# Kernel optimization log

Hardware: AMD Instinct MI355X
Metric: run time of the kernel (lower is better)

## Reference

```python
import jax, jax.numpy as jnp
import numpy as np

B, S, D, H = 2, 2048, 1024, 16
DK = D // H


def setup_inputs() -> dict:
    key = jax.random.key(0)
    ks = jax.random.split(key, 7)
    x = jax.random.normal(ks[0], (B, S, D), dtype=jnp.float32)
    gamma = jax.random.normal(ks[1], (D,), dtype=jnp.float32)
    mask = jax.random.randint(ks[2], (B, S), 0, 2, dtype=jnp.int32)
    w_qkv_w = jax.random.normal(ks[3], (D, 3 * D), dtype=jnp.float32) / np.sqrt(D)
    w_qkv_b = jax.random.normal(ks[4], (3 * D,), dtype=jnp.float32) * 0.02
    w_o_w = jax.random.normal(ks[5], (D, D), dtype=jnp.float32) / np.sqrt(D)
    w_o_b = jax.random.normal(ks[6], (D,), dtype=jnp.float32) * 0.02
    return {"x": x, "gamma": gamma, "mask": mask, "w_qkv_w": w_qkv_w,
            "w_qkv_b": w_qkv_b, "w_o_w": w_o_w, "w_o_b": w_o_b}


def reference(x, gamma, mask, w_qkv_w, w_qkv_b, w_o_w, w_o_b):
    b, s, d = x.shape
    # QKV projection, then per-head interleaved chunk (matches torch view+chunk)
    qkv = x @ w_qkv_w + w_qkv_b                      # [B,S,3D]
    qkv = qkv.reshape(b, s, H, 3 * DK).transpose(0, 2, 1, 3)  # [B,H,S,3*dk]
    q, k, v = jnp.split(qkv, 3, axis=-1)             # each [B,H,S,dk]
    scale = 1.0 / np.sqrt(DK).astype(np.float32)
    scores = jnp.einsum('bhqd,bhkd->bhqk', q, k) * scale  # [B,H,S,S]
    m = mask[:, None, None, :]                       # 2D mask -> [B,1,1,S]
    scores = jnp.where(m == 0, -jnp.inf, scores)
    attn = jax.nn.softmax(scores, axis=-1)           # dropout p=0.0 -> identity
    out = jnp.einsum('bhqk,bhkd->bhqd', attn, v)     # [B,H,S,dk]
    out = out.transpose(0, 2, 1, 3).reshape(b, s, d) # [B,S,D]
    out = out @ w_o_w + w_o_b
    return (gamma + 1.0) * out
```

## Files before the change

kernel.cpp:

```cpp
#include <hip/hip_runtime.h>
#include <hip/hip_bf16.h>


using bf16 = __hip_bfloat16;
typedef __attribute__((ext_vector_type(8))) short bf16x8;
typedef __attribute__((ext_vector_type(4))) float f32x4;

#define QSCALE 0.18033688011112042f

static __device__ __forceinline__ f32x4 mfma_bf16(bf16x8 a, bf16x8 b, f32x4 c) {
    return __builtin_amdgcn_mfma_f32_16x16x32_bf16(a, b, c, 0, 0, 0);
}

static __device__ __forceinline__ void gld_lds16(const void* g, void* s) {
    __builtin_amdgcn_global_load_lds(
        (const __attribute__((address_space(1))) unsigned int*)g,
        (__attribute__((address_space(3))) unsigned int*)s,
        16, 0, 0);
}

__global__ void cast_bf16_kernel(const float* __restrict__ in, bf16* __restrict__ out, int n4) {
    int i = blockIdx.x * blockDim.x + threadIdx.x;
    if (i >= n4) return;
    float4 f = reinterpret_cast<const float4*>(in)[i];
    out[4*i+0] = __float2bfloat16(f.x);
    out[4*i+1] = __float2bfloat16(f.y);
    out[4*i+2] = __float2bfloat16(f.z);
    out[4*i+3] = __float2bfloat16(f.w);
}

__global__ void transpose_cast_kernel(const float* __restrict__ in, bf16* __restrict__ out,
                                      int R, int C) {
    __shared__ float tile[32][33];
    int c0 = blockIdx.x * 32, r0 = blockIdx.y * 32;
    int x = threadIdx.x, y = threadIdx.y;
#pragma unroll
    for (int i = 0; i < 32; i += 8) tile[y + i][x] = in[(size_t)(r0 + y + i) * C + c0 + x];
    __syncthreads();
#pragma unroll
    for (int i = 0; i < 32; i += 8)
        out[(size_t)(c0 + y + i) * R + r0 + x] = __float2bfloat16(tile[x][y + i]);
}

template <int EPI>
__global__ __launch_bounds__(256, 2)
void gemm_bt_kernel(const bf16* __restrict__ A, const bf16* __restrict__ Bt,
                    int M, int N, int K,
                    const float* __restrict__ bias, const float* __restrict__ gamma,
                    bf16* __restrict__ Qout, bf16* __restrict__ Kout, bf16* __restrict__ Vtout,
                    float* __restrict__ Cout) {
    __shared__ __align__(16) bf16 As[128 * 64];
    __shared__ __align__(16) bf16 Bs[128 * 64];

    const int tid  = threadIdx.x;
    const int wave = tid >> 6, lane = tid & 63;
    const int quad = lane >> 4, l16 = lane & 15;
    const int wr = wave >> 1, wc = wave & 1;
    const int bm = blockIdx.y, bn = blockIdx.x;

    f32x4 acc[4][4] = {};

    const int crow = lane >> 3;
    const int sblk = (lane & 7) ^ (crow & 7);
    const bf16* gA[4]; const bf16* gB[4]; bf16* lA[4]; bf16* lB[4];
#pragma unroll
    for (int c = 0; c < 4; ++c) {
        int rt = wave * 32 + c * 8 + crow;
        gA[c] = A  + (size_t)(bm * 128 + rt) * K + sblk * 8;
        gB[c] = Bt + (size_t)(bn * 128 + rt) * K + sblk * 8;
        lA[c] = As + (wave * 4 + c) * 512 + lane * 8;
        lB[c] = Bs + (wave * 4 + c) * 512 + lane * 8;
    }
    const int xr = l16 & 7;

    for (int k0 = 0; k0 < K; k0 += 64) {
#pragma unroll
        for (int c = 0; c < 4; ++c) gld_lds16(gA[c] + k0, lA[c]);
#pragma unroll
        for (int c = 0; c < 4; ++c) gld_lds16(gB[c] + k0, lB[c]);
        __syncthreads();
#pragma unroll
        for (int ks = 0; ks < 2; ++ks) {
            bf16x8 af[4], bfr[4];
#pragma unroll
            for (int mi = 0; mi < 4; ++mi)
                af[mi] = *(const bf16x8*)(As + (wr * 64 + mi * 16 + l16) * 64 + ((4 * ks + quad) ^ xr) * 8);
#pragma unroll
            for (int ni = 0; ni < 4; ++ni)
                bfr[ni] = *(const bf16x8*)(Bs + (wc * 64 + ni * 16 + l16) * 64 + ((4 * ks + quad) ^ xr) * 8);
#pragma unroll
            for (int mi = 0; mi < 4; ++mi)
#pragma unroll
                for (int ni = 0; ni < 4; ++ni)
                    acc[mi][ni] = mfma_bf16(af[mi], bfr[ni], acc[mi][ni]);
        }
        __syncthreads();
    }

#pragma unroll
    for (int mi = 0; mi < 4; ++mi) {
#pragma unroll
        for (int ni = 0; ni < 4; ++ni) {
#pragma unroll
            for (int r = 0; r < 4; ++r) {
                int row = bm * 128 + wr * 64 + mi * 16 + quad * 4 + r;
                int col = bn * 128 + wc * 64 + ni * 16 + l16;
                float v = acc[mi][ni][r];
                if (EPI == 0) {
                    v += bias[col];
                    int h = col / 192;
                    int rr = col - h * 192;
                    int which = rr >> 6, dk = rr & 63;
                    int b = row >> 11, s = row & 2047;
                    size_t bh = (size_t)b * 16 + h;
                    if (which == 0) {
                        Qout[(bh * 2048 + s) * 64 + dk] = __float2bfloat16(v * QSCALE);
                    } else if (which == 1) {
                        Kout[(bh * 2048 + s) * 64 + dk] = __float2bfloat16(v);
                    } else {
                        Vtout[(bh * 64 + dk) * 2048 + s] = __float2bfloat16(v);
                    }
                } else {
                    float o = (gamma[col] + 1.0f) * (v + bias[col]);
                    Cout[(size_t)row * N + col] = o;
                }
            }
        }
    }
}

__global__ __launch_bounds__(256, 2)
void attn_kernel(const bf16* __restrict__ Qb, const bf16* __restrict__ Kb,
                 const bf16* __restrict__ Vt, const int* __restrict__ mask,
                 bf16* __restrict__ Aout) {
    __shared__ __align__(16) bf16 Ks[64 * 72];
    __shared__ __align__(16) bf16 Vs[64 * 72];
    __shared__ __align__(16) bf16 Ps[4][32 * 72];
    __shared__ float Biass[64];

    const int bh = blockIdx.y;
    const int b = bh >> 4, h = bh & 15;
    const int q0 = blockIdx.x * 128;
    const int tid = threadIdx.x;
    const int wave = tid >> 6, lane = tid & 63;
    const int quad = lane >> 4, l16 = lane & 15;

    bf16x8 aq[2][2];
#pragma unroll
    for (int m = 0; m < 2; ++m) {
        const bf16* qp = Qb + ((size_t)bh * 2048 + q0 + wave * 32 + m * 16 + l16) * 64;
        aq[m][0] = *(const bf16x8*)(qp + quad * 8);
        aq[m][1] = *(const bf16x8*)(qp + 32 + quad * 8);
    }

    bf16x8 ones;
#pragma unroll
    for (int j = 0; j < 8; ++j) ones[j] = (short)0x3F80;

    f32x4 O[2][4] = {};
    f32x4 Lacc[2] = {};

    const int srow = tid >> 2, spart = tid & 3;
    const bf16* gK = Kb + ((size_t)bh * 2048 + srow) * 64 + spart * 16;
    const bf16* gV = Vt + ((size_t)bh * 64 + srow) * 2048 + spart * 16;
    uint4* lK = (uint4*)(Ks + srow * 72 + spart * 16);
    uint4* lV = (uint4*)(Vs + srow * 72 + spart * 16);
    bf16* myPs = &Ps[wave][0];

    uint4 kr0, kr1, vr0, vr1; int mreg = 1;
    {
        const uint4* nk = (const uint4*)gK;
        const uint4* nv = (const uint4*)gV;
        kr0 = nk[0]; kr1 = nk[1];
        vr0 = nv[0]; vr1 = nv[1];
        if (tid < 64) mreg = mask[b * 2048 + tid];
    }

    for (int kt = 0; kt < 32; ++kt) {
        lK[0] = kr0; lK[1] = kr1;
        lV[0] = vr0; lV[1] = vr1;
        if (tid < 64) Biass[tid] = mreg ? -24.0f : -1e30f;
        __syncthreads();

        if (kt + 1 < 32) {
            const uint4* nk = (const uint4*)(gK + (size_t)(kt + 1) * 64 * 64);
            const uint4* nv = (const uint4*)(gV + (kt + 1) * 64);
            kr0 = nk[0]; kr1 = nk[1];
            vr0 = nv[0]; vr1 = nv[1];
            if (tid < 64) mreg = mask[b * 2048 + (kt + 1) * 64 + tid];
        }

        float bv4[4];
        bf16x8 bk[4][2];
#pragma unroll
        for (int nt = 0; nt < 4; ++nt) {
            bv4[nt] = Biass[nt * 16 + l16];
            const bf16* kp = Ks + (nt * 16 + l16) * 72 + quad * 8;
            bk[nt][0] = *(const bf16x8*)kp;
            bk[nt][1] = *(const bf16x8*)(kp + 32);
        }

#pragma unroll
        for (int m = 0; m < 2; ++m) {
#pragma unroll
            for (int nt = 0; nt < 4; ++nt) {
                f32x4 c = {0.f, 0.f, 0.f, 0.f};
                c = mfma_bf16(aq[m][0], bk[nt][0], c);
                c = mfma_bf16(aq[m][1], bk[nt][1], c);
#pragma unroll
                for (int r = 0; r < 4; ++r) {
                    float p = __builtin_amdgcn_exp2f(c[r] + bv4[nt]);
                    myPs[(m * 16 + quad * 4 + r) * 72 + nt * 16 + l16] = __float2bfloat16(p);
                }
            }
        }

#pragma unroll
        for (int m = 0; m < 2; ++m) {
#pragma unroll
            for (int ks = 0; ks < 2; ++ks) {
                bf16x8 ap = *(const bf16x8*)(myPs + (m * 16 + l16) * 72 + ks * 32 + quad * 8);
                Lacc[m] = mfma_bf16(ap, ones, Lacc[m]);
#pragma unroll
                for (int nt = 0; nt < 4; ++nt) {
                    bf16x8 bvv = *(const bf16x8*)(Vs + (nt * 16 + l16) * 72 + ks * 32 + quad * 8);
                    O[m][nt] = mfma_bf16(ap, bvv, O[m][nt]);
                }
            }
        }
        __syncthreads();
    }

#pragma unroll
    for (int m = 0; m < 2; ++m) {
        float inv[4];
#pragma unroll
        for (int r = 0; r < 4; ++r) inv[r] = __builtin_amdgcn_rcpf(Lacc[m][r]);
#pragma unroll
        for (int nt = 0; nt < 4; ++nt) {
#pragma unroll
            for (int r = 0; r < 4; ++r) {
                int row = q0 + wave * 32 + m * 16 + quad * 4 + r;
                Aout[((size_t)b * 2048 + row) * 1024 + h * 64 + nt * 16 + l16] =
                    __float2bfloat16(O[m][nt][r] * inv[r]);
            }
        }
    }
}

extern "C" void kernel_launch(void* const* d_in, const int* in_sizes, int n_in,
                              void* d_out, int out_size, void* d_ws, size_t ws_size,
                              hipStream_t stream) {
    const float* x     = (const float*)d_in[0];
    const float* gamma = (const float*)d_in[1];
    const int*   mask  = (const int*)d_in[2];
    const float* wqkv  = (const float*)d_in[3];
    const float* bqkv  = (const float*)d_in[4];
    const float* wo    = (const float*)d_in[5];
    const float* bo    = (const float*)d_in[6];
    float* out = (float*)d_out;

    char* ws = (char*)d_ws;
    const size_t MB = 1u << 20;
    bf16* xb    = (bf16*)(ws);
    bf16* wqkvT = (bf16*)(ws + 8 * MB);
    bf16* woT   = (bf16*)(ws + 14 * MB);
    bf16* Qb    = (bf16*)(ws + 16 * MB);
    bf16* Kb    = (bf16*)(ws + 24 * MB);
    bf16* Vt    = (bf16*)(ws + 32 * MB);
    bf16* attn  = (bf16*)(ws + 40 * MB);

    cast_bf16_kernel<<<4096, 256, 0, stream>>>(x, xb, 4194304 / 4);
    transpose_cast_kernel<<<dim3(96, 32), dim3(32, 8), 0, stream>>>(wqkv, wqkvT, 1024, 3072);
    transpose_cast_kernel<<<dim3(32, 32), dim3(32, 8), 0, stream>>>(wo, woT, 1024, 1024);

    gemm_bt_kernel<0><<<dim3(24, 32), 256, 0, stream>>>(
        xb, wqkvT, 4096, 3072, 1024, bqkv, nullptr, Qb, Kb, Vt, nullptr);

    attn_kernel<<<dim3(16, 32), 256, 0, stream>>>(Qb, Kb, Vt, mask, attn);

    gemm_bt_kernel<1><<<dim3(8, 32), 256, 0, stream>>>(
        attn, woT, 4096, 1024, 1024, bo, gamma, nullptr, nullptr, nullptr, out);
}
```

Baseline: 211.9 us.

## Stream K/V tiles via global_load_lds with XOR swizzle and separate V transpose

The QKV GEMM now writes V row-major, and a new kernel transposes it into Vt; this replaces the strided scattered transposed stores in the GEMM epilogue. The attention kernel loads K and V tiles straight into LDS with global_load_lds using an XOR swizzle instead of padded rows. It keeps P in fp32 LDS and packs to bf16 when reading, and hoists the V fragment loads out of the inner loop. The cost is an extra kernel launch and another round trip of V through memory. The register prefetch of the next tile is dropped, so loads are no longer overlapped with compute, and fp32 P doubles its LDS footprint.

```diff
diff --git a/kernel.cpp b/kernel.cpp
--- a/kernel.cpp
+++ b/kernel.cpp
@@ -17,6 +17,17 @@
         (const __attribute__((address_space(1))) unsigned int*)g,
         (__attribute__((address_space(3))) unsigned int*)s,
         16, 0, 0);
+}
+
+static __device__ __forceinline__ short f2s(float f) {
+    bf16 h = __float2bfloat16(f);
+    return *reinterpret_cast<short*>(&h);
+}
+static __device__ __forceinline__ bf16x8 pack8(float4 a, float4 b) {
+    bf16x8 r;
+    r[0] = f2s(a.x); r[1] = f2s(a.y); r[2] = f2s(a.z); r[3] = f2s(a.w);
+    r[4] = f2s(b.x); r[5] = f2s(b.y); r[6] = f2s(b.z); r[7] = f2s(b.w);
+    return r;
 }
 
 __global__ void cast_bf16_kernel(const float* __restrict__ in, bf16* __restrict__ out, int n4) {
@@ -42,12 +53,29 @@
         out[(size_t)(c0 + y + i) * R + r0 + x] = __float2bfloat16(tile[x][y + i]);
 }
 
+__global__ void transpose_v_kernel(const bf16* __restrict__ in, bf16* __restrict__ out) {
+    __shared__ bf16 t[64][72];
+    const int bh = blockIdx.y, s0 = blockIdx.x * 64;
+    const int r = threadIdx.x >> 2, c16 = (threadIdx.x & 3) * 16;
+    const uint4* src = (const uint4*)(in + ((size_t)bh * 2048 + s0 + r) * 64 + c16);
+    uint4 a = src[0], b = src[1];
+    *(uint4*)&t[r][c16] = a;
+    *(uint4*)&t[r][c16 + 8] = b;
+    __syncthreads();
+    bf16 tmp[16];
+#pragma unroll
+    for (int i = 0; i < 16; ++i) tmp[i] = t[c16 + i][r];
+    uint4* dst = (uint4*)(out + ((size_t)bh * 64 + r) * 2048 + s0 + c16);
+    dst[0] = ((uint4*)tmp)[0];
+    dst[1] = ((uint4*)tmp)[1];
+}
+
 template <int EPI>
 __global__ __launch_bounds__(256, 2)
 void gemm_bt_kernel(const bf16* __restrict__ A, const bf16* __restrict__ Bt,
                     int M, int N, int K,
                     const float* __restrict__ bias, const float* __restrict__ gamma,
-                    bf16* __restrict__ Qout, bf16* __restrict__ Kout, bf16* __restrict__ Vtout,
+                    bf16* __restrict__ Qout, bf16* __restrict__ Kout, bf16* __restrict__ Vout,
                     float* __restrict__ Cout) {
     __shared__ __align__(16) bf16 As[128 * 64];
     __shared__ __align__(16) bf16 Bs[128 * 64];
@@ -118,7 +146,7 @@
                     } else if (which == 1) {
                         Kout[(bh * 2048 + s) * 64 + dk] = __float2bfloat16(v);
                     } else {
-                        Vtout[(bh * 64 + dk) * 2048 + s] = __float2bfloat16(v);
+                        Vout[(bh * 2048 + s) * 64 + dk] = __float2bfloat16(v);
                     }
                 } else {
                     float o = (gamma[col] + 1.0f) * (v + bias[col]);
@@ -133,9 +161,9 @@
 void attn_kernel(const bf16* __restrict__ Qb, const bf16* __restrict__ Kb,
                  const bf16* __restrict__ Vt, const int* __restrict__ mask,
                  bf16* __restrict__ Aout) {
-    __shared__ __align__(16) bf16 Ks[64 * 72];
-    __shared__ __align__(16) bf16 Vs[64 * 72];
-    __shared__ __align__(16) bf16 Ps[4][32 * 72];
+    __shared__ __align__(16) bf16 Ks[64 * 64];
+    __shared__ __align__(16) bf16 Vs[64 * 64];
+    __shared__ __align__(16) float Psf[4][32 * 68];
     __shared__ float Biass[64];
 
     const int bh = blockIdx.y;
@@ -144,6 +172,7 @@
     const int tid = threadIdx.x;
     const int wave = tid >> 6, lane = tid & 63;
     const int quad = lane >> 4, l16 = lane & 15;
+    const int xr = l16 & 7;
 
     bf16x8 aq[2][2];
 #pragma unroll
@@ -160,44 +189,40 @@
     f32x4 O[2][4] = {};
     f32x4 Lacc[2] = {};
 
-    const int srow = tid >> 2, spart = tid & 3;
-    const bf16* gK = Kb + ((size_t)bh * 2048 + srow) * 64 + spart * 16;
-    const bf16* gV = Vt + ((size_t)bh * 64 + srow) * 2048 + spart * 16;
-    uint4* lK = (uint4*)(Ks + srow * 72 + spart * 16);
-    uint4* lV = (uint4*)(Vs + srow * 72 + spart * 16);
-    bf16* myPs = &Ps[wave][0];
-
-    uint4 kr0, kr1, vr0, vr1; int mreg = 1;
-    {
-        const uint4* nk = (const uint4*)gK;
-        const uint4* nv = (const uint4*)gV;
-        kr0 = nk[0]; kr1 = nk[1];
-        vr0 = nv[0]; vr1 = nv[1];
-        if (tid < 64) mreg = mask[b * 2048 + tid];
-    }
+    const int crow = lane >> 3;
+    const int sblk = (lane & 7) ^ (crow & 7);
+    const bf16* gK[2]; const bf16* gV[2]; bf16* lK[2]; bf16* lV[2];
+#pragma unroll
+    for (int c = 0; c < 2; ++c) {
+        int ch = wave * 2 + c;
+        gK[c] = Kb + ((size_t)bh * 2048 + ch * 8 + crow) * 64 + sblk * 8;
+        gV[c] = Vt + ((size_t)bh * 64 + ch * 8 + crow) * 2048 + sblk * 8;
+        lK[c] = Ks + ch * 512 + lane * 8;
+        lV[c] = Vs + ch * 512 + lane * 8;
+    }
+    float* myP = &Psf[wave][0];
+
+    int mreg = (tid < 64) ? mask[b * 2048 + tid] : 0;
 
     for (int kt = 0; kt < 32; ++kt) {
-        lK[0] = kr0; lK[1] = kr1;
-        lV[0] = vr0; lV[1] = vr1;
+#pragma unroll
+        for (int c = 0; c < 2; ++c) {
+            gld_lds16(gK[c] + (size_t)kt * 4096, lK[c]);
+            gld_lds16(gV[c] + kt * 64, lV[c]);
+        }
         if (tid < 64) Biass[tid] = mreg ? -24.0f : -1e30f;
         __syncthreads();
 
-        if (kt + 1 < 32) {
-            const uint4* nk = (const uint4*)(gK + (size_t)(kt + 1) * 64 * 64);
-            const uint4* nv = (const uint4*)(gV + (kt + 1) * 64);
-            kr0 = nk[0]; kr1 = nk[1];
-            vr0 = nv[0]; vr1 = nv[1];
-            if (tid < 64) mreg = mask[b * 2048 + (kt + 1) * 64 + tid];
-        }
+        if (kt + 1 < 32 && tid < 64) mreg = mask[b * 2048 + (kt + 1) * 64 + tid];
 
         float bv4[4];
         bf16x8 bk[4][2];
 #pragma unroll
         for (int nt = 0; nt < 4; ++nt) {
             bv4[nt] = Biass[nt * 16 + l16];
-            const bf16* kp = Ks + (nt * 16 + l16) * 72 + quad * 8;
-            bk[nt][0] = *(const bf16x8*)kp;
-            bk[nt][1] = *(const bf16x8*)(kp + 32);
+            const bf16* kp = Ks + (nt * 16 + l16) * 64;
+            bk[nt][0] = *(const bf16x8*)(kp + ((quad) ^ xr) * 8);
+            bk[nt][1] = *(const bf16x8*)(kp + ((quad + 4) ^ xr) * 8);
         }
 
 #pragma unroll
@@ -207,25 +232,31 @@
                 f32x4 c = {0.f, 0.f, 0.f, 0.f};
                 c = mfma_bf16(aq[m][0], bk[nt][0], c);
                 c = mfma_bf16(aq[m][1], bk[nt][1], c);
-#pragma unroll
-                for (int r = 0; r < 4; ++r) {
-                    float p = __builtin_amdgcn_exp2f(c[r] + bv4[nt]);
-                    myPs[(m * 16 + quad * 4 + r) * 72 + nt * 16 + l16] = __float2bfloat16(p);
-                }
+                float* pw = myP + (m * 16 + quad * 4) * 68 + nt * 16 + l16;
+#pragma unroll
+                for (int r = 0; r < 4; ++r)
+                    pw[r * 68] = __builtin_amdgcn_exp2f(c[r] + bv4[nt]);
             }
         }
 
+        bf16x8 bv[2][4];
+#pragma unroll
+        for (int ks = 0; ks < 2; ++ks)
+#pragma unroll
+            for (int nt = 0; nt < 4; ++nt)
+                bv[ks][nt] = *(const bf16x8*)(Vs + (nt * 16 + l16) * 64 + ((quad + 4 * ks) ^ xr) * 8);
+
 #pragma unroll
         for (int m = 0; m < 2; ++m) {
 #pragma unroll
             for (int ks = 0; ks < 2; ++ks) {
-                bf16x8 ap = *(const bf16x8*)(myPs + (m * 16 + l16) * 72 + ks * 32 + quad * 8);
+                const float4* pp = (const float4*)(myP + (m * 16 + l16) * 68 + ks * 32 + quad * 8);
+                float4 p0 = pp[0], p1 = pp[1];
+                bf16x8 ap = pack8(p0, p1);
                 Lacc[m] = mfma_bf16(ap, ones, Lacc[m]);
 #pragma unroll
-                for (int nt = 0; nt < 4; ++nt) {
-                    bf16x8 bvv = *(const bf16x8*)(Vs + (nt * 16 + l16) * 72 + ks * 32 + quad * 8);
-                    O[m][nt] = mfma_bf16(ap, bvv, O[m][nt]);
-                }
+                for (int nt = 0; nt < 4; ++nt)
+                    O[m][nt] = mfma_bf16(ap, bv[ks][nt], O[m][nt]);
             }
         }
         __syncthreads();
@@ -268,6 +299,7 @@
     bf16* Qb    = (bf16*)(ws + 16 * MB);
     bf16* Kb    = (bf16*)(ws + 24 * MB);
     bf16* Vt    = (bf16*)(ws + 32 * MB);
+    bf16* Vtmp  = (bf16*)(ws + 40 * MB);
     bf16* attn  = (bf16*)(ws + 40 * MB);
 
     cast_bf16_kernel<<<4096, 256, 0, stream>>>(x, xb, 4194304 / 4);
@@ -275,7 +307,9 @@
     transpose_cast_kernel<<<dim3(32, 32), dim3(32, 8), 0, stream>>>(wo, woT, 1024, 1024);
 
     gemm_bt_kernel<0><<<dim3(24, 32), 256, 0, stream>>>(
-        xb, wqkvT, 4096, 3072, 1024, bqkv, nullptr, Qb, Kb, Vt, nullptr);
+        xb, wqkvT, 4096, 3072, 1024, bqkv, nullptr, Qb, Kb, Vtmp, nullptr);
+
+    transpose_v_kernel<<<dim3(32, 32), 256, 0, stream>>>(Vtmp, Vt);
 
     attn_kernel<<<dim3(16, 32), 256, 0, stream>>>(Qb, Kb, Vt, mask, attn);
 
```

Result: no change. 215.5 us (+1.7%).

## Keep attention probabilities in registers and add separate V transpose kernel

Applied to the files above, without the earlier changes.

The attention kernel now computes S^T by swapping MFMA operands, so the exp'd probabilities already sit in the register layout needed as the A operand of the PV MFMA. This removes the per-wave LDS round trip for P and frees that shared memory. V fragments are gathered with 4-element loads from a padded LDS layout. Separately, the QKV GEMM now writes V row-major with coalesced stores and a new small kernel transposes it to V^T, which adds a launch and extra memory traffic in exchange for removing the strided scatter in the GEMM epilogue.

```diff
diff --git a/kernel.cpp b/kernel.cpp
--- a/kernel.cpp
+++ b/kernel.cpp
@@ -4,6 +4,7 @@
 
 using bf16 = __hip_bfloat16;
 typedef __attribute__((ext_vector_type(8))) short bf16x8;
+typedef __attribute__((ext_vector_type(4))) short bf16x4;
 typedef __attribute__((ext_vector_type(4))) float f32x4;
 
 #define QSCALE 0.18033688011112042f
@@ -17,6 +18,11 @@
         (const __attribute__((address_space(1))) unsigned int*)g,
         (__attribute__((address_space(3))) unsigned int*)s,
         16, 0, 0);
+}
+
+static __device__ __forceinline__ short f2s(float f) {
+    bf16 h = __float2bfloat16(f);
+    return *reinterpret_cast<short*>(&h);
 }
 
 __global__ void cast_bf16_kernel(const float* __restrict__ in, bf16* __restrict__ out, int n4) {
@@ -42,12 +48,29 @@
         out[(size_t)(c0 + y + i) * R + r0 + x] = __float2bfloat16(tile[x][y + i]);
 }
 
+__global__ void transpose_v_kernel(const bf16* __restrict__ in, bf16* __restrict__ out) {
+    __shared__ bf16 t[64][72];
+    const int bh = blockIdx.y, s0 = blockIdx.x * 64;
+    const int r = threadIdx.x >> 2, c16 = (threadIdx.x & 3) * 16;
+    const uint4* src = (const uint4*)(in + ((size_t)bh * 2048 + s0 + r) * 64 + c16);
+    uint4 a = src[0], b = src[1];
+    *(uint4*)&t[r][c16] = a;
+    *(uint4*)&t[r][c16 + 8] = b;
+    __syncthreads();
+    bf16 tmp[16];
+#pragma unroll
+    for (int i = 0; i < 16; ++i) tmp[i] = t[c16 + i][r];
+    uint4* dst = (uint4*)(out + ((size_t)bh * 64 + r) * 2048 + s0 + c16);
+    dst[0] = ((uint4*)tmp)[0];
+    dst[1] = ((uint4*)tmp)[1];
+}
+
 template <int EPI>
 __global__ __launch_bounds__(256, 2)
 void gemm_bt_kernel(const bf16* __restrict__ A, const bf16* __restrict__ Bt,
                     int M, int N, int K,
                     const float* __restrict__ bias, const float* __restrict__ gamma,
-                    bf16* __restrict__ Qout, bf16* __restrict__ Kout, bf16* __restrict__ Vtout,
+                    bf16* __restrict__ Qout, bf16* __restrict__ Kout, bf16* __restrict__ Vout,
                     float* __restrict__ Cout) {
     __shared__ __align__(16) bf16 As[128 * 64];
     __shared__ __align__(16) bf16 Bs[128 * 64];
@@ -118,7 +141,7 @@
                     } else if (which == 1) {
                         Kout[(bh * 2048 + s) * 64 + dk] = __float2bfloat16(v);
                     } else {
-                        Vtout[(bh * 64 + dk) * 2048 + s] = __float2bfloat16(v);
+                        Vout[(bh * 2048 + s) * 64 + dk] = __float2bfloat16(v);
                     }
                 } else {
                     float o = (gamma[col] + 1.0f) * (v + bias[col]);
@@ -134,9 +157,8 @@
                  const bf16* __restrict__ Vt, const int* __restrict__ mask,
                  bf16* __restrict__ Aout) {
     __shared__ __align__(16) bf16 Ks[64 * 72];
-    __shared__ __align__(16) bf16 Vs[64 * 72];
-    __shared__ __align__(16) bf16 Ps[4][32 * 72];
-    __shared__ float Biass[64];
+    __shared__ __align__(16) bf16 Vs[64 * 76];
+    __shared__ __align__(16) float Biass[64];
 
     const int bh = blockIdx.y;
     const int b = bh >> 4, h = bh & 15;
@@ -164,8 +186,7 @@
     const bf16* gK = Kb + ((size_t)bh * 2048 + srow) * 64 + spart * 16;
     const bf16* gV = Vt + ((size_t)bh * 64 + srow) * 2048 + spart * 16;
     uint4* lK = (uint4*)(Ks + srow * 72 + spart * 16);
-    uint4* lV = (uint4*)(Vs + srow * 72 + spart * 16);
-    bf16* myPs = &Ps[wave][0];
+    uint4* lV = (uint4*)(Vs + srow * 76 + spart * 16);
 
     uint4 kr0, kr1, vr0, vr1; int mreg = 1;
     {
@@ -190,42 +211,58 @@
             if (tid < 64) mreg = mask[b * 2048 + (kt + 1) * 64 + tid];
         }
 
-        float bv4[4];
+        f32x4 bias4[4];
         bf16x8 bk[4][2];
 #pragma unroll
-        for (int nt = 0; nt < 4; ++nt) {
-            bv4[nt] = Biass[nt * 16 + l16];
-            const bf16* kp = Ks + (nt * 16 + l16) * 72 + quad * 8;
-            bk[nt][0] = *(const bf16x8*)kp;
-            bk[nt][1] = *(const bf16x8*)(kp + 32);
+        for (int kt4 = 0; kt4 < 4; ++kt4) {
+            bias4[kt4] = *(const f32x4*)(Biass + kt4 * 16 + quad * 4);
+            const bf16* kp = Ks + (kt4 * 16 + l16) * 72 + quad * 8;
+            bk[kt4][0] = *(const bf16x8*)kp;
+            bk[kt4][1] = *(const bf16x8*)(kp + 32);
+        }
+        bf16x8 bv8[2][4];
+#pragma unroll
+        for (int a = 0; a < 2; ++a) {
+#pragma unroll
+            for (int nt = 0; nt < 4; ++nt) {
+                const bf16* vp = Vs + (nt * 16 + l16) * 76 + a * 32 + quad * 4;
+                bf16x4 lo = *(const bf16x4*)vp;
+                bf16x4 hi = *(const bf16x4*)(vp + 16);
+                bf16x8 f;
+                f[0] = lo[0]; f[1] = lo[1]; f[2] = lo[2]; f[3] = lo[3];
+                f[4] = hi[0]; f[5] = hi[1]; f[6] = hi[2]; f[7] = hi[3];
+                bv8[a][nt] = f;
+            }
         }
 
 #pragma unroll
         for (int m = 0; m < 2; ++m) {
-#pragma unroll
-            for (int nt = 0; nt < 4; ++nt) {
+            f32x4 sv[4];
+#pragma unroll
+            for (int kt4 = 0; kt4 < 4; ++kt4) {
                 f32x4 c = {0.f, 0.f, 0.f, 0.f};
-                c = mfma_bf16(aq[m][0], bk[nt][0], c);
-                c = mfma_bf16(aq[m][1], bk[nt][1], c);
-#pragma unroll
-                for (int r = 0; r < 4; ++r) {
-                    float p = __builtin_amdgcn_exp2f(c[r] + bv4[nt]);
-                    myPs[(m * 16 + quad * 4 + r) * 72 + nt * 16 + l16] = __float2bfloat16(p);
-                }
-            }
-        }
-
-#pragma unroll
-        for (int m = 0; m < 2; ++m) {
-#pragma unroll
-            for (int ks = 0; ks < 2; ++ks) {
-                bf16x8 ap = *(const bf16x8*)(myPs + (m * 16 + l16) * 72 + ks * 32 + quad * 8);
-                Lacc[m] = mfma_bf16(ap, ones, Lacc[m]);
-#pragma unroll
-                for (int nt = 0; nt < 4; ++nt) {
-                    bf16x8 bvv = *(const bf16x8*)(Vs + (nt * 16 + l16) * 72 + ks * 32 + quad * 8);
-                    O[m][nt] = mfma_bf16(ap, bvv, O[m][nt]);
-                }
+                c = mfma_bf16(bk[kt4][0], aq[m][0], c);
+                c = mfma_bf16(bk[kt4][1], aq[m][1], c);
+                sv[kt4] = c;
+            }
+            float p[4][4];
+#pragma unroll
+            for (int kt4 = 0; kt4 < 4; ++kt4)
+#pragma unroll
+                for (int r = 0; r < 4; ++r)
+                    p[kt4][r] = __builtin_amdgcn_exp2f(sv[kt4][r] + bias4[kt4][r]);
+
+#pragma unroll
+            for (int a = 0; a < 2; ++a) {
+                bf16x8 pa;
+                pa[0] = f2s(p[2*a][0]);   pa[1] = f2s(p[2*a][1]);
+                pa[2] = f2s(p[2*a][2]);   pa[3] = f2s(p[2*a][3]);
+                pa[4] = f2s(p[2*a+1][0]); pa[5] = f2s(p[2*a+1][1]);
+                pa[6] = f2s(p[2*a+1][2]); pa[7] = f2s(p[2*a+1][3]);
+                Lacc[m] = mfma_bf16(pa, ones, Lacc[m]);
+#pragma unroll
+                for (int nt = 0; nt < 4; ++nt)
+                    O[m][nt] = mfma_bf16(pa, bv8[a][nt], O[m][nt]);
             }
         }
         __syncthreads();
@@ -268,6 +305,7 @@
     bf16* Qb    = (bf16*)(ws + 16 * MB);
     bf16* Kb    = (bf16*)(ws + 24 * MB);
     bf16* Vt    = (bf16*)(ws + 32 * MB);
+    bf16* Vtmp  = (bf16*)(ws + 40 * MB);
     bf16* attn  = (bf16*)(ws + 40 * MB);
 
     cast_bf16_kernel<<<4096, 256, 0, stream>>>(x, xb, 4194304 / 4);
@@ -275,7 +313,9 @@
     transpose_cast_kernel<<<dim3(32, 32), dim3(32, 8), 0, stream>>>(wo, woT, 1024, 1024);
 
     gemm_bt_kernel<0><<<dim3(24, 32), 256, 0, stream>>>(
-        xb, wqkvT, 4096, 3072, 1024, bqkv, nullptr, Qb, Kb, Vt, nullptr);
+        xb, wqkvT, 4096, 3072, 1024, bqkv, nullptr, Qb, Kb, Vtmp, nullptr);
+
+    transpose_v_kernel<<<dim3(32, 32), 256, 0, stream>>>(Vtmp, Vt);
 
     attn_kernel<<<dim3(16, 32), 256, 0, stream>>>(Qb, Kb, Vt, mask, attn);
 
```

Measured after the change: 209.4 us. About the same (-1.2%).
